# Kernel tuning notes

Measured on AMD Instinct MI355X. Metric: run time of the kernel, lower is better.

Reference implementation:

```python
import jax, jax.numpy as jnp
import numpy as np


def setup_inputs() -> dict:
    key = jax.random.key(0)
    k_x, k_w, k_W, k_b, k_idx = jax.random.split(key, 5)
    B, C, N, K, O = 2, 32, 40962, 25, 64
    x = jax.random.normal(k_x, (B, C, N), dtype=jnp.float32)
    neigh_weights = jax.random.uniform(k_w, (N, K, 3), dtype=jnp.float32)
    W = jax.random.normal(k_W, (O, K * C), dtype=jnp.float32) * 0.02
    b = jax.random.normal(k_b, (O,), dtype=jnp.float32) * 0.02
    neigh_indices = jax.random.randint(k_idx, (N, K, 3), 0, N, dtype=jnp.int32)
    return {"x": x, "neigh_weights": neigh_weights, "W": W, "b": b,
            "neigh_indices": neigh_indices}


def reference(x, neigh_weights, W, b, neigh_indices):
    # x: (B, C, N); neigh_indices/neigh_weights: (N, K, 3); W: (O, C*K); b: (O,)
    B, C, N = x.shape
    _, K, _ = neigh_indices.shape
    # Gather neighbor features: (B, C, N, K, 3)
    mat = x[:, :, neigh_indices]
    # Barycentric weighted sum over the 3 triangle vertices -> (B, C, N, K)
    s = jnp.einsum('bcnkt,nkt->bcnk', mat, neigh_weights)
    # Permute to (B, N, C, K) and apply Linear(C*K -> O)
    feat = s.transpose(0, 2, 1, 3).reshape(B * N, C * K)
    out = feat @ W.T + b  # (B*N, O)
    out = out.reshape(B, N, -1).transpose(0, 2, 1)  # (B, O, N)
    return out
```

## Files before the change

### kernel.cpp

```cpp
#include <hip/hip_runtime.h>
#include <hip/hip_fp16.h>

typedef __attribute__((ext_vector_type(8))) _Float16 half8;
typedef __attribute__((ext_vector_type(4))) float f32x4;

union U2H2 { unsigned int u; __half2 h; };

static __device__ __forceinline__ unsigned int pack2h(float a, float b) {
    U2H2 c; c.h = __floats2half2_rn(a, b); return c.u;
}
static __device__ __forceinline__ __half2 u_as_h2(unsigned int u) {
    U2H2 c; c.u = u; return c.h;
}
static __device__ __forceinline__ __half2 hi16(unsigned int u) {
    return u_as_h2(__builtin_amdgcn_perm(u, u, 0x03020302u));
}

#define SWZ(row, slot) ((slot) ^ ((row) & 3) ^ (((row) >> 2) & 3))

#define LDS_BARRIER()                                                \
    do {                                                             \
        asm volatile("s_waitcnt lgkmcnt(0)" ::: "memory");           \
        __builtin_amdgcn_s_barrier();                                \
        __builtin_amdgcn_sched_barrier(0);                           \
    } while (0)

__global__ __launch_bounds__(256) void prep_all(const float* __restrict__ x,
                                                const float* __restrict__ W,
                                                unsigned short* __restrict__ xth,
                                                unsigned short* __restrict__ Wrh,
                                                int N, int nT) {
    int bid = blockIdx.x, tid = threadIdx.x;
    if (bid >= nT) {
        int k = bid - nT;
#pragma unroll
        for (int it = 0; it < 8; ++it) {
            int r = tid + 256 * it;
            int o = r >> 5, c = r & 31;
            __half h = __float2half(W[o * 800 + c * 25 + k]);
            Wrh[k * 2048 + r] = *reinterpret_cast<unsigned short*>(&h);
        }
        return;
    }
    __shared__ float t[2][32][65];
    int n0 = bid * 64;
#pragma unroll
    for (int i = 0; i < 16; ++i) {
        int e = tid + 256 * i;
        int b = e >> 11, c = (e >> 6) & 31, nl = e & 63;
        int n = n0 + nl;
        t[b][c][nl] = (n < N) ? x[(size_t)(b * 32 + c) * N + n] : 0.f;
    }
    __syncthreads();
    int nl = tid >> 2, q = tid & 3, n = n0 + nl;
    if (n < N) {
#pragma unroll
        for (int b = 0; b < 2; ++b) {
            uint4 p;
            p.x = pack2h(t[b][q * 8 + 0][nl], t[b][q * 8 + 1][nl]);
            p.y = pack2h(t[b][q * 8 + 2][nl], t[b][q * 8 + 3][nl]);
            p.z = pack2h(t[b][q * 8 + 4][nl], t[b][q * 8 + 5][nl]);
            p.w = pack2h(t[b][q * 8 + 6][nl], t[b][q * 8 + 7][nl]);
            *reinterpret_cast<uint4*>(xth + (((size_t)b * N + n) * 32 + q * 8)) = p;
        }
    }
}

__global__ __launch_bounds__(256) void fused_main(
    const unsigned short* __restrict__ xth,
    const unsigned short* __restrict__ Wrh,
    const float* __restrict__ bias,
    const int* __restrict__ nidx,
    const float* __restrict__ nw,
    float* __restrict__ out,
    int N, int nt)
{
    __shared__ unsigned int idxw[64 * 75];
    __shared__ __align__(16) unsigned char sA[2][4096];
    __shared__ __align__(16) unsigned char sB[2][4096];

    const int bid = blockIdx.x;
    const int b0 = (bid & 7) >> 2;
    const int tile = (bid >> 3) * 4 + (bid & 3);
    if (tile >= nt) return;
    const int n0 = tile * 64;
    const int tid = threadIdx.x;

#pragma unroll
    for (int it = 0; it < 19; ++it) {
        int e = tid + 256 * it;
        if (e < 4800) {
            int n = n0 + e / 75;
            unsigned int u = 0;
            if (n < N) {
                size_t s = (size_t)n0 * 75 + e;
                int j = nidx[s];
                __half hw = __float2half(nw[s]);
                u = (unsigned int)j |
                    ((unsigned int)*reinterpret_cast<unsigned short*>(&hw) << 16);
            }
            idxw[e] = u;
        }
    }
    __syncthreads();

    const int row = tid >> 2;
    const int q   = tid & 3;
    const int wr_off = row * 64 + (SWZ(row, q) << 4);

    const int l = tid & 63, wv = tid >> 6, c16 = l & 15, g = l >> 4;
    const int arow = 16 * wv + c16;
    const int rd_a = arow * 64 + (SWZ(arow, g) << 4);

    const unsigned short* xb = xth + (size_t)b0 * N * 32 + q * 8;
    const unsigned int* iprow = &idxw[row * 75];

    unsigned int ru[3][3];
    uint4 rg[3][3];
    uint4 rB;

    f32x4 acc[4];
#pragma unroll
    for (int ot = 0; ot < 4; ++ot) acc[ot] = (f32x4){0.f, 0.f, 0.f, 0.f};

    rB = *reinterpret_cast<const uint4*>(Wrh + tid * 8);
#pragma unroll
    for (int kk = 0; kk < 3; ++kk)
#pragma unroll
        for (int t = 0; t < 3; ++t) ru[kk][t] = iprow[kk * 3 + t];
#pragma unroll
    for (int kk = 0; kk < 3; ++kk)
#pragma unroll
        for (int t = 0; t < 3; ++t)
            rg[kk][t] = *reinterpret_cast<const uint4*>(xb + (ru[kk][t] & 0xffffu) * 32);

#pragma unroll
    for (int k = 0; k < 25; ++k) {
        const int gb = k % 3, buf = k & 1;

        *reinterpret_cast<uint4*>(&sB[buf][wr_off]) = rB;
        if (k + 1 < 25)
            rB = *reinterpret_cast<const uint4*>(Wrh + (k + 1) * 2048 + tid * 8);

        {
            __half2 w0 = hi16(ru[gb][0]), w1 = hi16(ru[gb][1]), w2 = hi16(ru[gb][2]);
            uint4 v0 = rg[gb][0], v1 = rg[gb][1], v2 = rg[gb][2];
            uint4 p; U2H2 c;
            c.h = __hfma2(u_as_h2(v0.x), w0, __hfma2(u_as_h2(v1.x), w1, __hmul2(u_as_h2(v2.x), w2)));
            p.x = c.u;
            c.h = __hfma2(u_as_h2(v0.y), w0, __hfma2(u_as_h2(v1.y), w1, __hmul2(u_as_h2(v2.y), w2)));
            p.y = c.u;
            c.h = __hfma2(u_as_h2(v0.z), w0, __hfma2(u_as_h2(v1.z), w1, __hmul2(u_as_h2(v2.z), w2)));
            p.z = c.u;
            c.h = __hfma2(u_as_h2(v0.w), w0, __hfma2(u_as_h2(v1.w), w1, __hmul2(u_as_h2(v2.w), w2)));
            p.w = c.u;
            *reinterpret_cast<uint4*>(&sA[buf][wr_off]) = p;
        }

        if (k + 3 < 25) {
#pragma unroll
            for (int t = 0; t < 3; ++t) ru[gb][t] = iprow[(k + 3) * 3 + t];
        }

        LDS_BARRIER();

        if (k + 3 < 25) {
#pragma unroll
            for (int t = 0; t < 3; ++t)
                rg[gb][t] = *reinterpret_cast<const uint4*>(xb + (ru[gb][t] & 0xffffu) * 32);
        }

        {
            half8 af = *reinterpret_cast<const half8*>(&sA[buf][rd_a]);
            __builtin_amdgcn_s_setprio(1);
#pragma unroll
            for (int ot = 0; ot < 4; ++ot) {
                int orow = ot * 16 + c16;
                half8 bf = *reinterpret_cast<const half8*>(
                    &sB[buf][orow * 64 + (SWZ(orow, g) << 4)]);
                acc[ot] = __builtin_amdgcn_mfma_f32_16x16x32_f16(af, bf, acc[ot], 0, 0, 0);
            }
            __builtin_amdgcn_s_setprio(0);
        }
    }

#pragma unroll
    for (int ot = 0; ot < 4; ++ot) {
        int o = ot * 16 + c16;
        float bv = bias[o];
#pragma unroll
        for (int i = 0; i < 4; ++i) {
            int n = n0 + 16 * wv + 4 * g + i;
            if (n < N) out[((size_t)b0 * 64 + o) * N + n] = acc[ot][i] + bv;
        }
    }
}

extern "C" void kernel_launch(void* const* d_in, const int* in_sizes, int n_in,
                              void* d_out, int out_size, void* d_ws, size_t ws_size,
                              hipStream_t stream) {
    const float* x    = (const float*)d_in[0];
    const float* nw   = (const float*)d_in[1];
    const float* W    = (const float*)d_in[2];
    const float* bias = (const float*)d_in[3];
    const int*   nidx = (const int*)d_in[4];
    float* out = (float*)d_out;

    int N = in_sizes[0] / 64;

    unsigned short* xth = (unsigned short*)d_ws;
    unsigned short* Wrh = xth + (size_t)2 * N * 32;

    int nT = (N + 63) / 64;
    prep_all<<<nT + 25, 256, 0, stream>>>(x, W, xth, Wrh, N, nT);

    int nt = (N + 63) / 64;
    int grid = ((nt + 3) / 4) * 8;
    fused_main<<<grid, 256, 0, stream>>>(xth, Wrh, bias, nidx, nw, out, N, nt);
}
```

Measured before the change: 64.86 us.

## Stream neighbor indices/weights from global per thread and halve tile to 32 rows

Removes the LDS staging of the 64x75 index/weight table and its block-wide sync. Each thread now loads its own row's int3 indices and float3 weights directly from global memory, three k-steps ahead, and issues the x gathers before the barrier. The tile shrinks to 32 nodes with 128-thread blocks, which doubles the grid and cuts LDS use so more blocks can be resident. The cost is more global index traffic per thread, the W tile being loaded by half as many threads, and extra registers for the prefetch pipeline.

```diff
diff --git a/kernel.cpp b/kernel.cpp
--- a/kernel.cpp
+++ b/kernel.cpp
@@ -11,9 +11,6 @@
 }
 static __device__ __forceinline__ __half2 u_as_h2(unsigned int u) {
     U2H2 c; c.u = u; return c.h;
-}
-static __device__ __forceinline__ __half2 hi16(unsigned int u) {
-    return u_as_h2(__builtin_amdgcn_perm(u, u, 0x03020302u));
 }
 
 #define SWZ(row, slot) ((slot) ^ ((row) & 3) ^ (((row) >> 2) & 3))
@@ -66,7 +63,7 @@
     }
 }
 
-__global__ __launch_bounds__(256) void fused_main(
+__global__ __launch_bounds__(128) void fused_main(
     const unsigned short* __restrict__ xth,
     const unsigned short* __restrict__ Wrh,
     const float* __restrict__ bias,
@@ -75,75 +72,77 @@
     float* __restrict__ out,
     int N, int nt)
 {
-    __shared__ unsigned int idxw[64 * 75];
-    __shared__ __align__(16) unsigned char sA[2][4096];
+    __shared__ __align__(16) unsigned char sA[2][2048];
     __shared__ __align__(16) unsigned char sB[2][4096];
 
     const int bid = blockIdx.x;
     const int b0 = (bid & 7) >> 2;
     const int tile = (bid >> 3) * 4 + (bid & 3);
     if (tile >= nt) return;
-    const int n0 = tile * 64;
+    const int n0 = tile * 32;
     const int tid = threadIdx.x;
-
-#pragma unroll
-    for (int it = 0; it < 19; ++it) {
-        int e = tid + 256 * it;
-        if (e < 4800) {
-            int n = n0 + e / 75;
-            unsigned int u = 0;
-            if (n < N) {
-                size_t s = (size_t)n0 * 75 + e;
-                int j = nidx[s];
-                __half hw = __float2half(nw[s]);
-                u = (unsigned int)j |
-                    ((unsigned int)*reinterpret_cast<unsigned short*>(&hw) << 16);
-            }
-            idxw[e] = u;
-        }
-    }
-    __syncthreads();
 
     const int row = tid >> 2;
     const int q   = tid & 3;
+    const int nclamp = (n0 + row < N) ? (n0 + row) : (N - 1);
+    const int*   ib = nidx + (size_t)nclamp * 75;
+    const float* wb = nw   + (size_t)nclamp * 75;
+    const unsigned short* xb = xth + (size_t)b0 * N * 32 + q * 8;
+
     const int wr_off = row * 64 + (SWZ(row, q) << 4);
+
+    const int s1 = tid + 128;
+    const int sbo0 = (tid >> 2) * 64 + (SWZ((tid >> 2), (tid & 3)) << 4);
+    const int sbo1 = (s1 >> 2) * 64 + (SWZ((s1 >> 2), (s1 & 3)) << 4);
+    const int gbo0 = (tid >> 2) * 32 + (tid & 3) * 8;
+    const int gbo1 = (s1 >> 2) * 32 + (s1 & 3) * 8;
 
     const int l = tid & 63, wv = tid >> 6, c16 = l & 15, g = l >> 4;
     const int arow = 16 * wv + c16;
     const int rd_a = arow * 64 + (SWZ(arow, g) << 4);
 
-    const unsigned short* xb = xth + (size_t)b0 * N * 32 + q * 8;
-    const unsigned int* iprow = &idxw[row * 75];
-
-    unsigned int ru[3][3];
-    uint4 rg[3][3];
-    uint4 rB;
+    int3   ri[3];
+    float3 rw[3];
+    unsigned int rwh[3][3];
+    uint4  rg[3][3];
+    uint4  rB0, rB1;
 
     f32x4 acc[4];
 #pragma unroll
     for (int ot = 0; ot < 4; ++ot) acc[ot] = (f32x4){0.f, 0.f, 0.f, 0.f};
 
-    rB = *reinterpret_cast<const uint4*>(Wrh + tid * 8);
-#pragma unroll
-    for (int kk = 0; kk < 3; ++kk)
-#pragma unroll
-        for (int t = 0; t < 3; ++t) ru[kk][t] = iprow[kk * 3 + t];
-#pragma unroll
-    for (int kk = 0; kk < 3; ++kk)
-#pragma unroll
-        for (int t = 0; t < 3; ++t)
-            rg[kk][t] = *reinterpret_cast<const uint4*>(xb + (ru[kk][t] & 0xffffu) * 32);
+#pragma unroll
+    for (int kk = 0; kk < 3; ++kk) {
+        ri[kk] = *reinterpret_cast<const int3*>(ib + kk * 3);
+        rw[kk] = *reinterpret_cast<const float3*>(wb + kk * 3);
+    }
+#pragma unroll
+    for (int kk = 0; kk < 3; ++kk) {
+        rwh[kk][0] = pack2h(rw[kk].x, rw[kk].x);
+        rwh[kk][1] = pack2h(rw[kk].y, rw[kk].y);
+        rwh[kk][2] = pack2h(rw[kk].z, rw[kk].z);
+        rg[kk][0] = *reinterpret_cast<const uint4*>(xb + ri[kk].x * 32);
+        rg[kk][1] = *reinterpret_cast<const uint4*>(xb + ri[kk].y * 32);
+        rg[kk][2] = *reinterpret_cast<const uint4*>(xb + ri[kk].z * 32);
+        ri[kk] = *reinterpret_cast<const int3*>(ib + (kk + 3) * 3);
+        rw[kk] = *reinterpret_cast<const float3*>(wb + (kk + 3) * 3);
+    }
+    rB0 = *reinterpret_cast<const uint4*>(Wrh + gbo0);
+    rB1 = *reinterpret_cast<const uint4*>(Wrh + gbo1);
 
 #pragma unroll
     for (int k = 0; k < 25; ++k) {
         const int gb = k % 3, buf = k & 1;
 
-        *reinterpret_cast<uint4*>(&sB[buf][wr_off]) = rB;
-        if (k + 1 < 25)
-            rB = *reinterpret_cast<const uint4*>(Wrh + (k + 1) * 2048 + tid * 8);
+        *reinterpret_cast<uint4*>(&sB[buf][sbo0]) = rB0;
+        *reinterpret_cast<uint4*>(&sB[buf][sbo1]) = rB1;
+        if (k + 1 < 25) {
+            rB0 = *reinterpret_cast<const uint4*>(Wrh + (k + 1) * 2048 + gbo0);
+            rB1 = *reinterpret_cast<const uint4*>(Wrh + (k + 1) * 2048 + gbo1);
+        }
 
         {
-            __half2 w0 = hi16(ru[gb][0]), w1 = hi16(ru[gb][1]), w2 = hi16(ru[gb][2]);
+            __half2 w0 = u_as_h2(rwh[gb][0]), w1 = u_as_h2(rwh[gb][1]), w2 = u_as_h2(rwh[gb][2]);
             uint4 v0 = rg[gb][0], v1 = rg[gb][1], v2 = rg[gb][2];
             uint4 p; U2H2 c;
             c.h = __hfma2(u_as_h2(v0.x), w0, __hfma2(u_as_h2(v1.x), w1, __hmul2(u_as_h2(v2.x), w2)));
@@ -158,17 +157,19 @@
         }
 
         if (k + 3 < 25) {
-#pragma unroll
-            for (int t = 0; t < 3; ++t) ru[gb][t] = iprow[(k + 3) * 3 + t];
+            rwh[gb][0] = pack2h(rw[gb].x, rw[gb].x);
+            rwh[gb][1] = pack2h(rw[gb].y, rw[gb].y);
+            rwh[gb][2] = pack2h(rw[gb].z, rw[gb].z);
+            rg[gb][0] = *reinterpret_cast<const uint4*>(xb + ri[gb].x * 32);
+            rg[gb][1] = *reinterpret_cast<const uint4*>(xb + ri[gb].y * 32);
+            rg[gb][2] = *reinterpret_cast<const uint4*>(xb + ri[gb].z * 32);
+            if (k + 6 < 25) {
+                ri[gb] = *reinterpret_cast<const int3*>(ib + (k + 6) * 3);
+                rw[gb] = *reinterpret_cast<const float3*>(wb + (k + 6) * 3);
+            }
         }
 
         LDS_BARRIER();
-
-        if (k + 3 < 25) {
-#pragma unroll
-            for (int t = 0; t < 3; ++t)
-                rg[gb][t] = *reinterpret_cast<const uint4*>(xb + (ru[gb][t] & 0xffffu) * 32);
-        }
 
         {
             half8 af = *reinterpret_cast<const half8*>(&sA[buf][rd_a]);
@@ -214,7 +215,7 @@
     int nT = (N + 63) / 64;
     prep_all<<<nT + 25, 256, 0, stream>>>(x, W, xth, Wrh, N, nT);
 
-    int nt = (N + 63) / 64;
+    int nt = (N + 31) / 32;
     int grid = ((nt + 3) / 4) * 8;
-    fused_main<<<grid, 256, 0, stream>>>(xth, Wrh, bias, nidx, nw, out, N, nt);
-}
+    fused_main<<<grid, 128, 0, stream>>>(xth, Wrh, bias, nidx, nw, out, N, nt);
+}
```

Measured after the change: 88.23 us. 1.36x slower.

## Interleave both batches per node in xth and tile 32 nodes across batches

Applied to the files above, without the earlier changes.

The transposed fp16 x buffer now stores both batches side by side for each node (128 bytes contiguous per node), so one gathered neighbour index fetches both batches' channels. Each block handles 32 nodes times 2 batches as its 64 GEMM rows, which halves the index/weight staging per block and loads each neighbour index only once for both batches. The LDS swizzle gains an extra bit to keep bank-conflict avoidance for the new row mapping. The trade-off is more, smaller blocks and a changed output-store pattern split across batches.

```diff
diff --git a/kernel.cpp b/kernel.cpp
--- a/kernel.cpp
+++ b/kernel.cpp
@@ -16,7 +16,8 @@
     return u_as_h2(__builtin_amdgcn_perm(u, u, 0x03020302u));
 }
 
-#define SWZ(row, slot) ((slot) ^ ((row) & 3) ^ (((row) >> 2) & 3))
+#define SWZ(row, slot) \
+    ((slot) ^ ((row) & 3) ^ (((row) >> 2) & 3) ^ (((row) >> 5) & 1))
 
 #define LDS_BARRIER()                                                \
     do {                                                             \
@@ -61,7 +62,7 @@
             p.y = pack2h(t[b][q * 8 + 2][nl], t[b][q * 8 + 3][nl]);
             p.z = pack2h(t[b][q * 8 + 4][nl], t[b][q * 8 + 5][nl]);
             p.w = pack2h(t[b][q * 8 + 6][nl], t[b][q * 8 + 7][nl]);
-            *reinterpret_cast<uint4*>(xth + (((size_t)b * N + n) * 32 + q * 8)) = p;
+            *reinterpret_cast<uint4*>(xth + ((size_t)n * 64 + b * 32 + q * 8)) = p;
         }
     }
 }
@@ -73,23 +74,19 @@
     const int* __restrict__ nidx,
     const float* __restrict__ nw,
     float* __restrict__ out,
-    int N, int nt)
+    int N)
 {
-    __shared__ unsigned int idxw[64 * 75];
+    __shared__ unsigned int idxw[32 * 75];
     __shared__ __align__(16) unsigned char sA[2][4096];
     __shared__ __align__(16) unsigned char sB[2][4096];
 
-    const int bid = blockIdx.x;
-    const int b0 = (bid & 7) >> 2;
-    const int tile = (bid >> 3) * 4 + (bid & 3);
-    if (tile >= nt) return;
-    const int n0 = tile * 64;
     const int tid = threadIdx.x;
-
-#pragma unroll
-    for (int it = 0; it < 19; ++it) {
+    const int n0 = blockIdx.x * 32;
+
+#pragma unroll
+    for (int it = 0; it < 10; ++it) {
         int e = tid + 256 * it;
-        if (e < 4800) {
+        if (e < 2400) {
             int n = n0 + e / 75;
             unsigned int u = 0;
             if (n < N) {
@@ -104,16 +101,20 @@
     }
     __syncthreads();
 
-    const int row = tid >> 2;
-    const int q   = tid & 3;
-    const int wr_off = row * 64 + (SWZ(row, q) << 4);
+    const int nl = tid >> 3;
+    const int p  = tid & 7;
+    const int grow = (p >> 2) * 32 + nl;
+    const int q = p & 3;
+    const int wr_off = grow * 64 + (SWZ(grow, q) << 4);
+
+    const int sbo = (tid >> 2) * 64 + (SWZ((tid >> 2), (tid & 3)) << 4);
 
     const int l = tid & 63, wv = tid >> 6, c16 = l & 15, g = l >> 4;
     const int arow = 16 * wv + c16;
     const int rd_a = arow * 64 + (SWZ(arow, g) << 4);
 
-    const unsigned short* xb = xth + (size_t)b0 * N * 32 + q * 8;
-    const unsigned int* iprow = &idxw[row * 75];
+    const unsigned short* xg = xth + p * 8;
+    const unsigned int* iprow = &idxw[nl * 75];
 
     unsigned int ru[3][3];
     uint4 rg[3][3];
@@ -132,29 +133,29 @@
     for (int kk = 0; kk < 3; ++kk)
 #pragma unroll
         for (int t = 0; t < 3; ++t)
-            rg[kk][t] = *reinterpret_cast<const uint4*>(xb + (ru[kk][t] & 0xffffu) * 32);
+            rg[kk][t] = *reinterpret_cast<const uint4*>(xg + (ru[kk][t] & 0xffffu) * 64);
 
 #pragma unroll
     for (int k = 0; k < 25; ++k) {
         const int gb = k % 3, buf = k & 1;
 
-        *reinterpret_cast<uint4*>(&sB[buf][wr_off]) = rB;
+        *reinterpret_cast<uint4*>(&sB[buf][sbo]) = rB;
         if (k + 1 < 25)
             rB = *reinterpret_cast<const uint4*>(Wrh + (k + 1) * 2048 + tid * 8);
 
         {
             __half2 w0 = hi16(ru[gb][0]), w1 = hi16(ru[gb][1]), w2 = hi16(ru[gb][2]);
             uint4 v0 = rg[gb][0], v1 = rg[gb][1], v2 = rg[gb][2];
-            uint4 p; U2H2 c;
+            uint4 pk; U2H2 c;
             c.h = __hfma2(u_as_h2(v0.x), w0, __hfma2(u_as_h2(v1.x), w1, __hmul2(u_as_h2(v2.x), w2)));
-            p.x = c.u;
+            pk.x = c.u;
             c.h = __hfma2(u_as_h2(v0.y), w0, __hfma2(u_as_h2(v1.y), w1, __hmul2(u_as_h2(v2.y), w2)));
-            p.y = c.u;
+            pk.y = c.u;
             c.h = __hfma2(u_as_h2(v0.z), w0, __hfma2(u_as_h2(v1.z), w1, __hmul2(u_as_h2(v2.z), w2)));
-            p.z = c.u;
+            pk.z = c.u;
             c.h = __hfma2(u_as_h2(v0.w), w0, __hfma2(u_as_h2(v1.w), w1, __hmul2(u_as_h2(v2.w), w2)));
-            p.w = c.u;
-            *reinterpret_cast<uint4*>(&sA[buf][wr_off]) = p;
+            pk.w = c.u;
+            *reinterpret_cast<uint4*>(&sA[buf][wr_off]) = pk;
         }
 
         if (k + 3 < 25) {
@@ -167,7 +168,7 @@
         if (k + 3 < 25) {
 #pragma unroll
             for (int t = 0; t < 3; ++t)
-                rg[gb][t] = *reinterpret_cast<const uint4*>(xb + (ru[gb][t] & 0xffffu) * 32);
+                rg[gb][t] = *reinterpret_cast<const uint4*>(xg + (ru[gb][t] & 0xffffu) * 64);
         }
 
         {
@@ -190,8 +191,9 @@
         float bv = bias[o];
 #pragma unroll
         for (int i = 0; i < 4; ++i) {
-            int n = n0 + 16 * wv + 4 * g + i;
-            if (n < N) out[((size_t)b0 * 64 + o) * N + n] = acc[ot][i] + bv;
+            int mrow = 16 * wv + 4 * g + i;
+            int b = mrow >> 5, nn = n0 + (mrow & 31);
+            if (nn < N) out[((size_t)b * 64 + o) * N + nn] = acc[ot][i] + bv;
         }
     }
 }
@@ -209,12 +211,10 @@
     int N = in_sizes[0] / 64;
 
     unsigned short* xth = (unsigned short*)d_ws;
-    unsigned short* Wrh = xth + (size_t)2 * N * 32;
+    unsigned short* Wrh = xth + (size_t)N * 64;
 
     int nT = (N + 63) / 64;
     prep_all<<<nT + 25, 256, 0, stream>>>(x, W, xth, Wrh, N, nT);
 
-    int nt = (N + 63) / 64;
-    int grid = ((nt + 3) / 4) * 8;
-    fused_main<<<grid, 256, 0, stream>>>(xth, Wrh, bias, nidx, nw, out, N, nt);
-}
+    fused_main<<<(N + 31) / 32, 256, 0, stream>>>(xth, Wrh, bias, nidx, nw, out, N);
+}
```

Result: faster. 58.03 us (-10.5%).
